# Kernel optimization log

Measured on AMD Instinct MI355X. Metric: run time of the kernel, lower is better.

The kernel has to match this reference:

```python
import jax, jax.numpy as jnp
import numpy as np

ALPHA = 0.9   # LIF membrane decay
VTH = 1.0     # LIF threshold
H = 8         # attention heads
ACH = 0.5     # acetylcholine level for thalamic gate

# Heaviside spike with fast-sigmoid surrogate gradient (standard SNN trick)
@jax.custom_vjp
def spike(v):
    return (v >= 0.0).astype(v.dtype)

def _spike_fwd(v):
    return (v >= 0.0).astype(v.dtype), v

def _spike_bwd(v, g):
    return (g / (1.0 + 2.0 * jnp.abs(v)) ** 2,)

spike.defvjp(_spike_fwd, _spike_bwd)

def lif(x):
    """Leaky-integrate-and-fire over time. x: (B,T,D) -> spikes (B,T,D). Soft reset."""
    def step(u, xt):
        u = ALPHA * u + xt
        s = spike(u - VTH)
        return u - s * VTH, s
    u0 = jnp.zeros_like(x[:, 0])
    _, s = jax.lax.scan(step, u0, jnp.swapaxes(x, 0, 1))  # scan over T
    return jnp.swapaxes(s, 0, 1)

def rwkv_wkv(k, v, w_decay, u_first):
    """Numerically-stable RWKV time-mixing recurrence. k,v: (B,T,D) -> wkv (B,T,D)."""
    w = jnp.exp(w_decay)  # positive per-channel decay
    def step(carry, kv):
        aa, bb, pp = carry
        kt, vt = kv
        ww = u_first + kt
        p = jnp.maximum(pp, ww)
        e1 = jnp.exp(pp - p); e2 = jnp.exp(ww - p)
        wkv = (e1 * aa + e2 * vt) / (e1 * bb + e2)
        ww2 = pp - w
        p2 = jnp.maximum(ww2, kt)
        e1 = jnp.exp(ww2 - p2); e2 = jnp.exp(kt - p2)
        return (e1 * aa + e2 * vt, e1 * bb + e2, p2), wkv
    B, T, D = k.shape
    init = (jnp.zeros((B, D), k.dtype), jnp.zeros((B, D), k.dtype),
            jnp.full((B, D), -1e30, k.dtype))
    _, wkv = jax.lax.scan(step, init, (jnp.swapaxes(k, 0, 1), jnp.swapaxes(v, 0, 1)))
    return jnp.swapaxes(wkv, 0, 1)


def setup_inputs() -> dict:
    key = jax.random.key(0)
    B, T, D = 4, 1024, 1024
    ks = jax.random.split(key, 16)
    s = 1.0 / np.sqrt(D)
    def W(k):
        return jax.random.normal(k, (D, D), jnp.float32) * s
    return {
        "x": jax.random.normal(ks[0], (B, T, D), jnp.float32),
        "context": jax.random.normal(ks[1], (B, T, D), jnp.float32),
        "Wg": W(ks[2]), "bg": jnp.zeros((D,), jnp.float32), "Wc": W(ks[3]),
        "Wq": W(ks[4]), "Wk": W(ks[5]), "Wv": W(ks[6]), "Wo": W(ks[7]),
        "Wm": W(ks[8]),
        "rWk": W(ks[9]), "rWv": W(ks[10]), "rWr": W(ks[11]), "rWo": W(ks[12]),
        "w_decay": jax.random.normal(ks[13], (D,), jnp.float32) * 0.1,
        "u_first": jax.random.normal(ks[14], (D,), jnp.float32) * 0.1,
        "gamma": jnp.ones((D,), jnp.float32), "beta": jnp.zeros((D,), jnp.float32),
    }


def reference(x, context, Wg, bg, Wc, Wq, Wk, Wv, Wo, Wm, rWk, rWv, rWr, rWo,
              w_decay, u_first, gamma, beta):
    B, T, D = x.shape
    dh = D // H
    # stage 1: thalamic gate (ach interpolates between pass-through and gated)
    gate = jax.nn.sigmoid(x @ Wg + bg + context @ Wc)
    gated = x * (ACH * gate + (1.0 - ACH))
    # stage 2: LIF integration (sequential over T)
    spikes2 = lif(gated)
    # stage 3: spike self-attention
    q = (spikes2 @ Wq).reshape(B, T, H, dh)
    k = (spikes2 @ Wk).reshape(B, T, H, dh)
    v = (spikes2 @ Wv).reshape(B, T, H, dh)
    scores = jnp.einsum('bthd,bshd->bhts', q, k) / np.sqrt(dh).astype(np.float32)
    attn = jax.nn.softmax(scores, axis=-1)
    attn_out = jnp.einsum('bhts,bshd->bthd', attn, v).reshape(B, T, D) @ Wo
    # stage 4: apical modulation by top-down context
    modulated = attn_out * (1.0 + jnp.tanh(context @ Wm))
    # stage 5: RWKV recurrence
    r = jax.nn.sigmoid(modulated @ rWr)
    wkv = rwkv_wkv(modulated @ rWk, modulated @ rWv, w_decay, u_first)
    recurrent = (r * wkv) @ rWo
    # stage 6: output LIF + residual + LayerNorm
    y = lif(recurrent) + spikes2
    mu = jnp.mean(y, axis=-1, keepdims=True)
    var = jnp.var(y, axis=-1, keepdims=True)
    return (y - mu) * jax.lax.rsqrt(var + 1e-5) * gamma + beta
```

## Files before the change

kernel.cpp:

```cpp
#include <hip/hip_runtime.h>
#include <hip/hip_bf16.h>
#include <math.h>

#define BDIM 4
#define TDIM 1024
#define DDIM 1024
#define DH   128
#define NELEM ((size_t)BDIM * TDIM * DDIM)

typedef __attribute__((ext_vector_type(8))) _Float16 hfrag;
typedef __attribute__((ext_vector_type(4))) float facc;

__device__ __forceinline__ void split2(float x, ushort& h1, ushort& h2) {
  const _Float16 a = (_Float16)x;
  const _Float16 b = (_Float16)((x - (float)a) * 2048.0f);
  union { _Float16 h; ushort u; } ua, ub;
  ua.h = a; ub.h = b;
  h1 = ua.u; h2 = ub.u;
}
#define INV2048 4.8828125e-4f

__device__ __forceinline__ float fexp(float x) {
  return __builtin_amdgcn_exp2f(x * 1.4426950408889634f);
}

constexpr int GM = 4096, GN = 1024, GK = 1024;
constexpr int BM = 128, BK = 32;
constexpr int BKP = 40;

__global__ __launch_bounds__(256)
void cvt_h2t(const float* __restrict__ W0, const float* __restrict__ W1,
             const float* __restrict__ W2, ushort* __restrict__ P,
             int zstride, int zkoff, int kTot) {
  __shared__ float Ls[64][68];
  const int z = blockIdx.z;
  const float* W = (z == 0) ? W0 : (z == 1 ? W1 : W2);
  ushort* Pz = P + (size_t)z * zstride;
  const size_t PS = (size_t)kTot * GN;
  const int t = threadIdx.x;
  const int k0 = blockIdx.x * 64, n0 = blockIdx.y * 64;
  const int r = t >> 4, c4 = (t & 15) << 2;
#pragma unroll
  for (int i = 0; i < 4; ++i)
    *(float4*)&Ls[r + i * 16][c4] =
        *(const float4*)(W + (size_t)(k0 + r + i * 16) * GN + n0 + c4);
  __syncthreads();
  const int n = t >> 2, kc = (t & 3) << 4;
  uint p1[8], p2[8];
#pragma unroll
  for (int jj = 0; jj < 8; ++jj) {
    const float x0 = Ls[kc + 2 * jj][n], x1 = Ls[kc + 2 * jj + 1][n];
    ushort a1, a2, b1, b2;
    split2(x0, a1, a2);
    split2(x1, b1, b2);
    p1[jj] = (uint)a1 | ((uint)b1 << 16);
    p2[jj] = (uint)a2 | ((uint)b2 << 16);
  }
  const int kk = k0 + kc + z * zkoff;
  ushort* d = Pz + (size_t)(kk >> 5) * (GN * 32) + (size_t)(n0 + n) * 32 + (kk & 31);
  *(uint4*)(d)          = *(uint4*)&p1[0];
  *(uint4*)(d + 8)      = *(uint4*)&p1[4];
  *(uint4*)(d + PS)     = *(uint4*)&p2[0];
  *(uint4*)(d + PS + 8) = *(uint4*)&p2[4];
}

template<int EPI, int AU8, int KTOT, int GATE>
__global__ __launch_bounds__(256)
void gemm_k(const void* __restrict__ A0, const void* __restrict__ A1,
            const void* __restrict__ A2, const void* __restrict__ Ak2,
            const ushort* __restrict__ pB,
            float* __restrict__ C0, float* __restrict__ C1,
            float* __restrict__ C2,
            const float* __restrict__ xg, const float* __restrict__ bgv) {
  constexpr size_t PS = (size_t)KTOT * GN;
  __shared__ ushort As[2][BM][BKP];
  __shared__ ushort Bs[2][64][BKP];
  const int tid = threadIdx.x;
  const int n   = blockIdx.x;
  const int xcd = n & 7;
  const int idx = n >> 3;
  const int by  = xcd * 4 + (idx & 3);
  const int bx  = idx >> 2;
  const int mat = bx >> 4;
  const int row0 = by * BM;
  const int col0 = (bx & 15) * 64;
  const ushort* pBm = pB + (size_t)mat * 2 * PS;
  float* C = (mat == 0) ? C0 : (mat == 1 ? C1 : C2);
  const void* Abase = (mat == 0) ? A0 : (mat == 1 ? A1 : A2);

  const int sm  = tid & 127;
  const int sk0 = (tid >> 7) << 4;

  const int wave = tid >> 6;
  const int lane = tid & 63;
  const int wrow = (wave >> 1) * 64;
  const int wcol = (wave & 1) * 32;
  const int lrow = lane & 15;
  const int kof  = (lane >> 4) * 8;

  facc accM[4][2], accS[4][2];
#pragma unroll
  for (int i = 0; i < 4; ++i)
#pragma unroll
    for (int j = 0; j < 2; ++j) { accM[i][j] = (facc)0.f; accS[i][j] = (facc)0.f; }

  float av[16];
  uint4 a8raw;
  uint4 bregs[2];

  auto gloadA = [&](int K0) {
    const void* src = Abase; int k = K0;
    if (KTOT > 1024 && K0 >= 1024) { src = Ak2; k = K0 - 1024; }
    if (AU8) {
      a8raw = *(const uint4*)((const uint8_t*)src + (size_t)(row0 + sm) * 1024 + k + sk0);
    } else {
      const float* Ap = (const float*)src + (size_t)(row0 + sm) * 1024 + k + sk0;
      *(float4*)&av[0]  = *(const float4*)(Ap);
      *(float4*)&av[4]  = *(const float4*)(Ap + 4);
      *(float4*)&av[8]  = *(const float4*)(Ap + 8);
      *(float4*)&av[12] = *(const float4*)(Ap + 12);
    }
  };
  auto gloadB = [&](int K0) {
    const int kb = K0 >> 5;
#pragma unroll
    for (int j = 0; j < 2; ++j) {
      const int u = tid + 256 * j;
      const int q = u & 3, nn = (u >> 2) & 63, p = u >> 8;
      bregs[j] = *(const uint4*)(pBm + (size_t)p * PS + (size_t)kb * (GN * 32)
                                 + (size_t)(col0 + nn) * 32 + q * 8);
    }
  };
  auto swrite = [&]() {
    if (AU8) {
      const uint w4[4] = {a8raw.x, a8raw.y, a8raw.z, a8raw.w};
      uint pk[8];
#pragma unroll
      for (int i = 0; i < 8; ++i) {
        const uint b0 = (w4[i >> 1] >> ((i & 1) * 16)) & 0xFFu;
        const uint b1 = (w4[i >> 1] >> ((i & 1) * 16 + 8)) & 0xFFu;
        pk[i] = (b0 * 0x3C00u) | ((b1 * 0x3C00u) << 16);
      }
      *(uint4*)&As[0][sm][sk0]     = *(uint4*)&pk[0];
      *(uint4*)&As[0][sm][sk0 + 8] = *(uint4*)&pk[4];
    } else {
      uint q1[8], q2[8];
#pragma unroll
      for (int i = 0; i < 8; ++i) {
        ushort a1, a2, b1, b2;
        split2(av[2 * i], a1, a2);
        split2(av[2 * i + 1], b1, b2);
        q1[i] = (uint)a1 | ((uint)b1 << 16);
        q2[i] = (uint)a2 | ((uint)b2 << 16);
      }
      *(uint4*)&As[0][sm][sk0]     = *(uint4*)&q1[0];
      *(uint4*)&As[0][sm][sk0 + 8] = *(uint4*)&q1[4];
      *(uint4*)&As[1][sm][sk0]     = *(uint4*)&q2[0];
      *(uint4*)&As[1][sm][sk0 + 8] = *(uint4*)&q2[4];
    }
#pragma unroll
    for (int j = 0; j < 2; ++j) {
      const int u = tid + 256 * j;
      const int q = u & 3, nn = (u >> 2) & 63, p = u >> 8;
      *(uint4*)&Bs[p][nn][q * 8] = bregs[j];
    }
  };

  gloadA(0); gloadB(0);
  for (int k0 = 0; k0 < KTOT; k0 += BK) {
    __syncthreads();
    swrite();
    const int kn = k0 + BK;
    if (kn < KTOT) { gloadA(kn); gloadB(kn); }
    __syncthreads();
    hfrag fb1[2], fb2[2];
#pragma unroll
    for (int f = 0; f < 2; ++f) {
      fb1[f] = *(const hfrag*)&Bs[0][wcol + f * 16 + lrow][kof];
      fb2[f] = *(const hfrag*)&Bs[1][wcol + f * 16 + lrow][kof];
    }
#pragma unroll
    for (int mi = 0; mi < 4; ++mi) {
      const hfrag a1 = *(const hfrag*)&As[0][wrow + mi * 16 + lrow][kof];
      hfrag a2;
      if (!AU8) a2 = *(const hfrag*)&As[1][wrow + mi * 16 + lrow][kof];
#pragma unroll
      for (int ni = 0; ni < 2; ++ni)
        accM[mi][ni] = __builtin_amdgcn_mfma_f32_16x16x32_f16(a1, fb1[ni], accM[mi][ni], 0, 0, 0);
#pragma unroll
      for (int ni = 0; ni < 2; ++ni) {
        accS[mi][ni] = __builtin_amdgcn_mfma_f32_16x16x32_f16(a1, fb2[ni], accS[mi][ni], 0, 0, 0);
        if (!AU8)
          accS[mi][ni] = __builtin_amdgcn_mfma_f32_16x16x32_f16(a2, fb1[ni], accS[mi][ni], 0, 0, 0);
      }
    }
  }

#pragma unroll
  for (int mi = 0; mi < 4; ++mi) {
#pragma unroll
    for (int ni = 0; ni < 2; ++ni) {
      const int rbase = row0 + wrow + mi * 16 + (lane >> 4) * 4;
      const int cc    = col0 + wcol + ni * 16 + lrow;
      float* cp = C + (size_t)rbase * GN + cc;
#pragma unroll
      for (int r = 0; r < 4; ++r) {
        float v = accM[mi][ni][r] + accS[mi][ni][r] * INV2048;
        if (EPI == 1) v += cp[(size_t)r * GN];
        if (GATE == 1) {
          const float xv = xg[(size_t)(rbase + r) * GN + cc];
          const float s  = 1.0f / (1.0f + expf(-(v + bgv[cc])));
          v = xv * (0.5f * s + 0.5f);
        }
        cp[(size_t)r * GN] = v;
      }
    }
  }
}

__device__ __forceinline__ float sigf(float z) { return 1.0f / (1.0f + expf(-z)); }

__global__ __launch_bounds__(256)
void mod_kernel(const float* __restrict__ a, const float* __restrict__ c,
                float* __restrict__ out) {
  const int i4 = blockIdx.x * 256 + threadIdx.x;
  const float4 av = ((const float4*)a)[i4];
  const float4 cv = ((const float4*)c)[i4];
  float4 r;
  r.x = av.x * (1.0f + tanhf(cv.x));
  r.y = av.y * (1.0f + tanhf(cv.y));
  r.z = av.z * (1.0f + tanhf(cv.z));
  r.w = av.w * (1.0f + tanhf(cv.w));
  ((float4*)out)[i4] = r;
}

__global__ __launch_bounds__(256)
void rmul_kernel(const float* __restrict__ rr, const float* __restrict__ wkv,
                 float* __restrict__ out) {
  const int i4 = blockIdx.x * 256 + threadIdx.x;
  const float4 rv = ((const float4*)rr)[i4];
  const float4 wv = ((const float4*)wkv)[i4];
  float4 r;
  r.x = sigf(rv.x) * wv.x;
  r.y = sigf(rv.y) * wv.y;
  r.z = sigf(rv.z) * wv.z;
  r.w = sigf(rv.w) * wv.w;
  ((float4*)out)[i4] = r;
}

__global__ __launch_bounds__(64)
void lif_u8_kernel(const float* __restrict__ x, uint8_t* __restrict__ s) {
  const int c = blockIdx.x * 64 + threadIdx.x;
  const size_t off = (size_t)(c >> 10) * TDIM * DDIM + (c & 1023);
  const float* xp = x + off;
  uint8_t* sp = s + off;
  float u = 0.f;
  float cur[32];
#pragma unroll
  for (int i = 0; i < 32; ++i) cur[i] = xp[(size_t)i * DDIM];
  for (int t = 0; t < TDIM; t += 32) {
    float nxt[32];
    if (t + 32 < TDIM) {
#pragma unroll
      for (int i = 0; i < 32; ++i) nxt[i] = xp[(size_t)(t + 32 + i) * DDIM];
    }
#pragma unroll
    for (int i = 0; i < 32; ++i) {
      u = __fadd_rn(__fmul_rn(0.9f, u), cur[i]);
      const bool fire = (u >= 1.0f);
      sp[(size_t)(t + i) * DDIM] = fire ? 1 : 0;
      if (fire) u -= 1.0f;
    }
#pragma unroll
    for (int i = 0; i < 32; ++i) cur[i] = nxt[i];
  }
}

__global__ __launch_bounds__(64)
void lif_ip_kernel(float* __restrict__ x) {
  const int c = blockIdx.x * 64 + threadIdx.x;
  const size_t off = (size_t)(c >> 10) * TDIM * DDIM + (c & 1023);
  float* xp = x + off;
  float u = 0.f;
  float cur[32];
#pragma unroll
  for (int i = 0; i < 32; ++i) cur[i] = xp[(size_t)i * DDIM];
  for (int t = 0; t < TDIM; t += 32) {
    float nxt[32];
    if (t + 32 < TDIM) {
#pragma unroll
      for (int i = 0; i < 32; ++i) nxt[i] = xp[(size_t)(t + 32 + i) * DDIM];
    }
#pragma unroll
    for (int i = 0; i < 32; ++i) {
      u = __fadd_rn(__fmul_rn(0.9f, u), cur[i]);
      const float sv = (u >= 1.0f) ? 1.0f : 0.0f;
      xp[(size_t)(t + i) * DDIM] = sv;
      u -= sv;
    }
#pragma unroll
    for (int i = 0; i < 32; ++i) cur[i] = nxt[i];
  }
}

__global__ __launch_bounds__(64)
void rwkv_kernel(const float* __restrict__ k, const float* __restrict__ v,
                 const float* __restrict__ wd, const float* __restrict__ uf,
                 float* __restrict__ out) {
  const int c = blockIdx.x * 64 + threadIdx.x;
  const int d = c & 1023;
  const size_t off = (size_t)(c >> 10) * TDIM * DDIM + d;
  const float* kp = k + off;
  const float* vp = v + off;
  float* op = out + off;
  const float w = expf(wd[d]);
  const float u = uf[d];
  float aa = 0.f, bb = 0.f, pp = -1e30f;
  float kc[16], vc[16];
#pragma unroll
  for (int i = 0; i < 16; ++i) {
    kc[i] = kp[(size_t)i * DDIM];
    vc[i] = vp[(size_t)i * DDIM];
  }
  for (int t = 0; t < TDIM; t += 16) {
    float kn[16], vn[16];
    if (t + 16 < TDIM) {
#pragma unroll
      for (int i = 0; i < 16; ++i) {
        kn[i] = kp[(size_t)(t + 16 + i) * DDIM];
        vn[i] = vp[(size_t)(t + 16 + i) * DDIM];
      }
    }
#pragma unroll
    for (int i = 0; i < 16; ++i) {
      const float kt = kc[i], vt = vc[i];
      const float ww = __fadd_rn(u, kt);
      const float p  = fmaxf(pp, ww);
      float e1 = fexp(__fsub_rn(pp, p));
      float e2 = fexp(__fsub_rn(ww, p));
      const float num = __fadd_rn(__fmul_rn(e1, aa), __fmul_rn(e2, vt));
      const float den = __fadd_rn(__fmul_rn(e1, bb), e2);
      op[(size_t)(t + i) * DDIM] = num * __builtin_amdgcn_rcpf(den);
      const float ww2 = __fsub_rn(pp, w);
      const float p2  = fmaxf(ww2, kt);
      e1 = fexp(__fsub_rn(ww2, p2));
      e2 = fexp(__fsub_rn(kt, p2));
      aa = __fadd_rn(__fmul_rn(e1, aa), __fmul_rn(e2, vt));
      bb = __fadd_rn(__fmul_rn(e1, bb), e2);
      pp = p2;
    }
#pragma unroll
    for (int i = 0; i < 16; ++i) { kc[i] = kn[i]; vc[i] = vn[i]; }
  }
}

__global__ __launch_bounds__(256)
void flash_attn(const float* __restrict__ Q, const float* __restrict__ K,
                const float* __restrict__ V, float* __restrict__ O) {
  __shared__ ushort Ks[2][32][136];
  __shared__ ushort Vt[2][128][40];
  __shared__ ushort Pl[4][2][16][40];
  const int tid = threadIdx.x;
  const int n    = blockIdx.x;
  const int xcd  = n & 7;
  const int idx  = n >> 3;
  const int qt   = idx & 15;
  const int grp4 = idx >> 4;
  const int p    = grp4 * 8 + xcd;
  const int b    = p >> 3, h = p & 7;
  const size_t base = ((size_t)b * TDIM) * DDIM + (size_t)h * DH;

  const int wave = tid >> 6;
  const int lane = tid & 63;
  const int lr   = lane & 15;
  const int g    = lane >> 4;
  const int sr   = tid >> 3;
  const int sc   = (tid & 7) * 16;
  const int vslot = (sr + 8 * (tid & 3)) & 31;

  hfrag q1[4], q2[4];
  {
    const float* Qrow = Q + base + (size_t)(qt * 64 + wave * 16 + lr) * DDIM;
#pragma unroll
    for (int s = 0; s < 4; ++s) {
      const float4 f0 = *(const float4*)(Qrow + s * 32 + g * 8);
      const float4 f1 = *(const float4*)(Qrow + s * 32 + g * 8 + 4);
      const float qf[8] = {f0.x, f0.y, f0.z, f0.w, f1.x, f1.y, f1.z, f1.w};
      union { hfrag v; ushort u[8]; } u1, u2;
#pragma unroll
      for (int j = 0; j < 8; ++j) split2(qf[j], u1.u[j], u2.u[j]);
      q1[s] = u1.v; q2[s] = u2.v;
    }
  }

  facc oM[8], oS[8];
#pragma unroll
  for (int i = 0; i < 8; ++i) { oM[i] = (facc)0.f; oS[i] = (facc)0.f; }
  float m[4] = {-INFINITY, -INFINITY, -INFINITY, -INFINITY};
  float l[4] = {0.f, 0.f, 0.f, 0.f};
  const float ISC = 0.08838834764831845f;

  float kv[16], vv[16];
  auto gload = [&](int kt0) {
    const float* Kg = K + base + (size_t)(kt0 + sr) * DDIM + sc;
    const float* Vg = V + base + (size_t)(kt0 + sr) * DDIM + sc;
    *(float4*)&kv[0]  = *(const float4*)(Kg);
    *(float4*)&kv[4]  = *(const float4*)(Kg + 4);
    *(float4*)&kv[8]  = *(const float4*)(Kg + 8);
    *(float4*)&kv[12] = *(const float4*)(Kg + 12);
    *(float4*)&vv[0]  = *(const float4*)(Vg);
    *(float4*)&vv[4]  = *(const float4*)(Vg + 4);
    *(float4*)&vv[8]  = *(const float4*)(Vg + 8);
    *(float4*)&vv[12] = *(const float4*)(Vg + 12);
  };
  gload(0);

  for (int kt0 = 0; kt0 < TDIM; kt0 += 32) {
    __syncthreads();
    {
      uint w1[8], w2[8];
#pragma unroll
      for (int i = 0; i < 8; ++i) {
        ushort a1, a2, b1, b2;
        split2(kv[2 * i], a1, a2);
        split2(kv[2 * i + 1], b1, b2);
        w1[i] = (uint)a1 | ((uint)b1 << 16);
        w2[i] = (uint)a2 | ((uint)b2 << 16);
      }
      *(uint4*)&Ks[0][sr][sc]     = *(uint4*)&w1[0];
      *(uint4*)&Ks[0][sr][sc + 8] = *(uint4*)&w1[4];
      *(uint4*)&Ks[1][sr][sc]     = *(uint4*)&w2[0];
      *(uint4*)&Ks[1][sr][sc + 8] = *(uint4*)&w2[4];
#pragma unroll
      for (int i = 0; i < 16; ++i) {
        ushort a1, a2;
        split2(vv[i], a1, a2);
        Vt[0][sc + i][vslot] = a1;
        Vt[1][sc + i][vslot] = a2;
      }
    }
    if (kt0 + 32 < TDIM) gload(kt0 + 32);
    __syncthreads();

    facc sM0 = (facc)0.f, sS0 = (facc)0.f, sM1 = (facc)0.f, sS1 = (facc)0.f;
#pragma unroll
    for (int s = 0; s < 4; ++s) {
      const int ko = s * 32 + g * 8;
      const hfrag kb10 = *(const hfrag*)&Ks[0][lr][ko];
      const hfrag kb11 = *(const hfrag*)&Ks[0][lr + 16][ko];
      const hfrag kb20 = *(const hfrag*)&Ks[1][lr][ko];
      const hfrag kb21 = *(const hfrag*)&Ks[1][lr + 16][ko];
      sM0 = __builtin_amdgcn_mfma_f32_16x16x32_f16(q1[s], kb10, sM0, 0, 0, 0);
      sS0 = __builtin_amdgcn_mfma_f32_16x16x32_f16(q1[s], kb20, sS0, 0, 0, 0);
      sS0 = __builtin_amdgcn_mfma_f32_16x16x32_f16(q2[s], kb10, sS0, 0, 0, 0);
      sM1 = __builtin_amdgcn_mfma_f32_16x16x32_f16(q1[s], kb11, sM1, 0, 0, 0);
      sS1 = __builtin_amdgcn_mfma_f32_16x16x32_f16(q1[s], kb21, sS1, 0, 0, 0);
      sS1 = __builtin_amdgcn_mfma_f32_16x16x32_f16(q2[s], kb11, sS1, 0, 0, 0);
    }

#pragma unroll
    for (int r = 0; r < 4; ++r) {
      const float sc0 = (sM0[r] + sS0[r] * INV2048) * ISC;
      const float sc1 = (sM1[r] + sS1[r] * INV2048) * ISC;
      float mx = fmaxf(sc0, sc1);
      mx = fmaxf(mx, __shfl_xor(mx, 1, 16));
      mx = fmaxf(mx, __shfl_xor(mx, 2, 16));
      mx = fmaxf(mx, __shfl_xor(mx, 4, 16));
      mx = fmaxf(mx, __shfl_xor(mx, 8, 16));
      const float mn = fmaxf(m[r], mx);
      const float rf = fexp(m[r] - mn);
      const float p0 = fexp(sc0 - mn), p1 = fexp(sc1 - mn);
      float ps = p0 + p1;
      ps += __shfl_xor(ps, 1, 16);
      ps += __shfl_xor(ps, 2, 16);
      ps += __shfl_xor(ps, 4, 16);
      ps += __shfl_xor(ps, 8, 16);
      l[r] = l[r] * rf + ps;
      m[r] = mn;
#pragma unroll
      for (int nf = 0; nf < 8; ++nf) { oM[nf][r] *= rf; oS[nf][r] *= rf; }
      ushort a1, a2;
      split2(p0, a1, a2);
      Pl[wave][0][g * 4 + r][lr] = a1;
      Pl[wave][1][g * 4 + r][lr] = a2;
      split2(p1, a1, a2);
      Pl[wave][0][g * 4 + r][lr + 16] = a1;
      Pl[wave][1][g * 4 + r][lr + 16] = a2;
    }

    const hfrag pa1 = *(const hfrag*)&Pl[wave][0][lr][g * 8];
    const hfrag pa2 = *(const hfrag*)&Pl[wave][1][lr][g * 8];
#pragma unroll
    for (int nf = 0; nf < 8; ++nf) {
      const int vs = 8 * ((g + nf) & 3);
      const hfrag vb1 = *(const hfrag*)&Vt[0][nf * 16 + lr][vs];
      const hfrag vb2 = *(const hfrag*)&Vt[1][nf * 16 + lr][vs];
      oM[nf] = __builtin_amdgcn_mfma_f32_16x16x32_f16(pa1, vb1, oM[nf], 0, 0, 0);
      oS[nf] = __builtin_amdgcn_mfma_f32_16x16x32_f16(pa1, vb2, oS[nf], 0, 0, 0);
      oS[nf] = __builtin_amdgcn_mfma_f32_16x16x32_f16(pa2, vb1, oS[nf], 0, 0, 0);
    }
  }

  float* Og = O + base + (size_t)(qt * 64 + wave * 16) * DDIM;
#pragma unroll
  for (int r = 0; r < 4; ++r) {
    const float invl = 1.0f / l[r];
    float* orow = Og + (size_t)(g * 4 + r) * DDIM;
#pragma unroll
    for (int nf = 0; nf < 8; ++nf)
      orow[nf * 16 + lr] = (oM[nf][r] + oS[nf][r] * INV2048) * invl;
  }
}

__global__ __launch_bounds__(256)
void ln_kernel(const float* __restrict__ a, const uint8_t* __restrict__ s8,
               const float* __restrict__ gamma, const float* __restrict__ beta,
               float* __restrict__ out) {
  const int row = blockIdx.x;
  const int tid = threadIdx.x;
  const size_t base = (size_t)row * DDIM;
  const float4 av = *(const float4*)(a + base + tid * 4);
  const uchar4 sv = *(const uchar4*)(s8 + base + tid * 4);
  const float y0 = av.x + (float)sv.x, y1 = av.y + (float)sv.y;
  const float y2 = av.z + (float)sv.z, y3 = av.w + (float)sv.w;
  float s = (y0 + y1) + (y2 + y3);
  float q = (y0 * y0 + y1 * y1) + (y2 * y2 + y3 * y3);
#pragma unroll
  for (int off = 1; off < 64; off <<= 1) {
    s += __shfl_xor(s, off);
    q += __shfl_xor(q, off);
  }
  __shared__ float red[8];
  const int wid = tid >> 6;
  if ((tid & 63) == 0) { red[wid * 2] = s; red[wid * 2 + 1] = q; }
  __syncthreads();
  const float ts = (red[0] + red[2]) + (red[4] + red[6]);
  const float tq = (red[1] + red[3]) + (red[5] + red[7]);
  const float mu  = ts * (1.0f / 1024.0f);
  const float var = tq * (1.0f / 1024.0f) - mu * mu;
  const float rs  = 1.0f / sqrtf(var + 1e-5f);
  const int d = tid * 4;
  const float4 gv  = *(const float4*)(gamma + d);
  const float4 btv = *(const float4*)(beta + d);
  float4 r;
  r.x = (y0 - mu) * rs * gv.x + btv.x;
  r.y = (y1 - mu) * rs * gv.y + btv.y;
  r.z = (y2 - mu) * rs * gv.z + btv.z;
  r.w = (y3 - mu) * rs * gv.w + btv.w;
  *(float4*)(out + base + d) = r;
}

extern "C" void kernel_launch(void* const* d_in, const int* in_sizes, int n_in,
                              void* d_out, int out_size, void* d_ws, size_t ws_size,
                              hipStream_t stream) {
  const float* x       = (const float*)d_in[0];
  const float* context = (const float*)d_in[1];
  const float* Wg  = (const float*)d_in[2];
  const float* bg  = (const float*)d_in[3];
  const float* Wc  = (const float*)d_in[4];
  const float* Wq  = (const float*)d_in[5];
  const float* Wk  = (const float*)d_in[6];
  const float* Wv  = (const float*)d_in[7];
  const float* Wo  = (const float*)d_in[8];
  const float* Wm  = (const float*)d_in[9];
  const float* rWk = (const float*)d_in[10];
  const float* rWv = (const float*)d_in[11];
  const float* rWr = (const float*)d_in[12];
  const float* rWo = (const float*)d_in[13];
  const float* wd  = (const float*)d_in[14];
  const float* uf  = (const float*)d_in[15];
  const float* gamma = (const float*)d_in[16];
  const float* beta  = (const float*)d_in[17];
  float* out = (float*)d_out;

  float* w  = (float*)d_ws;
  float*   bA = w;
  float*   bC = w + 1 * NELEM;
  float*   bD = w + 2 * NELEM;
  float*   bE = w + 3 * NELEM;
  uint8_t* bS = (uint8_t*)(w + 4 * NELEM);
  ushort*  pB = (ushort*)((uint8_t*)d_ws + 4 * NELEM * 4 + NELEM);

  const dim3 ew(4096);
  constexpr int M1 = 1024 * 1024;

  cvt_h2t<<<dim3(16, 16, 2), 256, 0, stream>>>(Wg, Wc, nullptr, pB, 0, 1024, 2048);
  gemm_k<0, 0, 2048, 1><<<512, 256, 0, stream>>>(x, nullptr, nullptr, context,
                                                 pB, bA, nullptr, nullptr, x, bg);
  lif_u8_kernel<<<64, 64, 0, stream>>>(bA, bS);
  cvt_h2t<<<dim3(16, 16, 3), 256, 0, stream>>>(Wq, Wk, Wv, pB, 2 * M1, 0, 1024);
  gemm_k<0, 1, 1024, 0><<<1536, 256, 0, stream>>>(bS, bS, bS, nullptr, pB,
                                                  bA, bC, bD, nullptr, nullptr);
  flash_attn<<<512, 256, 0, stream>>>(bA, bC, bD, bA);
  cvt_h2t<<<dim3(16, 16, 2), 256, 0, stream>>>(Wo, Wm, nullptr, pB, 2 * M1, 0, 1024);
  gemm_k<0, 0, 1024, 0><<<1024, 256, 0, stream>>>(bA, context, nullptr, nullptr,
                                                  pB, bC, bE, nullptr,
                                                  nullptr, nullptr);
  mod_kernel<<<ew, 256, 0, stream>>>(bC, bE, bD);
  cvt_h2t<<<dim3(16, 16, 3), 256, 0, stream>>>(rWk, rWv, rWr, pB, 2 * M1, 0, 1024);
  gemm_k<0, 0, 1024, 0><<<1536, 256, 0, stream>>>(bD, bD, bD, nullptr, pB,
                                                  bA, bC, bE, nullptr, nullptr);
  rwkv_kernel<<<64, 64, 0, stream>>>(bA, bC, wd, uf, bA);
  rmul_kernel<<<ew, 256, 0, stream>>>(bE, bA, bA);
  cvt_h2t<<<dim3(16, 16, 1), 256, 0, stream>>>(rWo, nullptr, nullptr, pB, 0, 0, 1024);
  gemm_k<0, 0, 1024, 0><<<512, 256, 0, stream>>>(bA, nullptr, nullptr, nullptr,
                                                 pB, bC, nullptr, nullptr,
                                                 nullptr, nullptr);
  lif_ip_kernel<<<64, 64, 0, stream>>>(bC);
  ln_kernel<<<4096, 256, 0, stream>>>(bC, bS, gamma, beta, out);
}
```

Measured before the change: 967.2 us.

## Double-buffer GEMM global prefetch registers to hide load latency

The GEMM main loop now keeps two sets of prefetch registers for the A and B tiles and unrolls the K loop by two. Global loads are issued two BK steps ahead instead of one, so memory latency has more time to overlap with MFMA compute. In exchange the kernel holds more registers, which may lower occupancy. The change also assumes KTOT is a multiple of 2*BK.

Result: no change. 966.1 us (-0.1%).

```diff
diff --git a/kernel.cpp b/kernel.cpp
--- a/kernel.cpp
+++ b/kernel.cpp
@@ -104,36 +104,36 @@
 #pragma unroll
     for (int j = 0; j < 2; ++j) { accM[i][j] = (facc)0.f; accS[i][j] = (facc)0.f; }
 
-  float av[16];
-  uint4 a8raw;
-  uint4 bregs[2];
-
-  auto gloadA = [&](int K0) {
+  float av0[16], av1[16];
+  uint4 a80, a81;
+  uint4 br0[2], br1[2];
+
+  auto gloadA = [&](int K0, float* avd, uint4& a8d) {
     const void* src = Abase; int k = K0;
     if (KTOT > 1024 && K0 >= 1024) { src = Ak2; k = K0 - 1024; }
     if (AU8) {
-      a8raw = *(const uint4*)((const uint8_t*)src + (size_t)(row0 + sm) * 1024 + k + sk0);
+      a8d = *(const uint4*)((const uint8_t*)src + (size_t)(row0 + sm) * 1024 + k + sk0);
     } else {
       const float* Ap = (const float*)src + (size_t)(row0 + sm) * 1024 + k + sk0;
-      *(float4*)&av[0]  = *(const float4*)(Ap);
-      *(float4*)&av[4]  = *(const float4*)(Ap + 4);
-      *(float4*)&av[8]  = *(const float4*)(Ap + 8);
-      *(float4*)&av[12] = *(const float4*)(Ap + 12);
+      *(float4*)&avd[0]  = *(const float4*)(Ap);
+      *(float4*)&avd[4]  = *(const float4*)(Ap + 4);
+      *(float4*)&avd[8]  = *(const float4*)(Ap + 8);
+      *(float4*)&avd[12] = *(const float4*)(Ap + 12);
     }
   };
-  auto gloadB = [&](int K0) {
+  auto gloadB = [&](int K0, uint4* bd) {
     const int kb = K0 >> 5;
 #pragma unroll
     for (int j = 0; j < 2; ++j) {
       const int u = tid + 256 * j;
       const int q = u & 3, nn = (u >> 2) & 63, p = u >> 8;
-      bregs[j] = *(const uint4*)(pBm + (size_t)p * PS + (size_t)kb * (GN * 32)
-                                 + (size_t)(col0 + nn) * 32 + q * 8);
+      bd[j] = *(const uint4*)(pBm + (size_t)p * PS + (size_t)kb * (GN * 32)
+                              + (size_t)(col0 + nn) * 32 + q * 8);
     }
   };
-  auto swrite = [&]() {
+  auto swrite = [&](const float* avs, const uint4& a8s, const uint4* bs) {
     if (AU8) {
-      const uint w4[4] = {a8raw.x, a8raw.y, a8raw.z, a8raw.w};
+      const uint w4[4] = {a8s.x, a8s.y, a8s.z, a8s.w};
       uint pk[8];
 #pragma unroll
       for (int i = 0; i < 8; ++i) {
@@ -148,8 +148,8 @@
 #pragma unroll
       for (int i = 0; i < 8; ++i) {
         ushort a1, a2, b1, b2;
-        split2(av[2 * i], a1, a2);
-        split2(av[2 * i + 1], b1, b2);
+        split2(avs[2 * i], a1, a2);
+        split2(avs[2 * i + 1], b1, b2);
         q1[i] = (uint)a1 | ((uint)b1 << 16);
         q2[i] = (uint)a2 | ((uint)b2 << 16);
       }
@@ -162,17 +162,10 @@
     for (int j = 0; j < 2; ++j) {
       const int u = tid + 256 * j;
       const int q = u & 3, nn = (u >> 2) & 63, p = u >> 8;
-      *(uint4*)&Bs[p][nn][q * 8] = bregs[j];
+      *(uint4*)&Bs[p][nn][q * 8] = bs[j];
     }
   };
-
-  gloadA(0); gloadB(0);
-  for (int k0 = 0; k0 < KTOT; k0 += BK) {
-    __syncthreads();
-    swrite();
-    const int kn = k0 + BK;
-    if (kn < KTOT) { gloadA(kn); gloadB(kn); }
-    __syncthreads();
+  auto compute = [&]() {
     hfrag fb1[2], fb2[2];
 #pragma unroll
     for (int f = 0; f < 2; ++f) {
@@ -194,6 +187,21 @@
           accS[mi][ni] = __builtin_amdgcn_mfma_f32_16x16x32_f16(a2, fb1[ni], accS[mi][ni], 0, 0, 0);
       }
     }
+  };
+
+  gloadA(0, av0, a80);  gloadB(0, br0);
+  gloadA(BK, av1, a81); gloadB(BK, br1);
+  for (int k0 = 0; k0 < KTOT; k0 += 2 * BK) {
+    __syncthreads();
+    swrite(av0, a80, br0);
+    if (k0 + 2 * BK < KTOT) { gloadA(k0 + 2 * BK, av0, a80); gloadB(k0 + 2 * BK, br0); }
+    __syncthreads();
+    compute();
+    __syncthreads();
+    swrite(av1, a81, br1);
+    if (k0 + 3 * BK < KTOT) { gloadA(k0 + 3 * BK, av1, a81); gloadB(k0 + 3 * BK, br1); }
+    __syncthreads();
+    compute();
   }
 
 #pragma unroll
```

## Double-buffer LDS tiles in split-fp16 GEMM to halve barriers per K step

Applied to the files above, without the earlier changes.

Shared-memory A and B tiles become double-buffered, so each iteration writes the next stage into the alternate buffer while the MFMA computes on the current one. This cuts the synchronisations per K-step from two to one and prefetches global loads two stages ahead. The cost is doubled LDS use and more live registers, which may lower occupancy.

Result: faster. 862.9 us, median of 2 (-10.8%).

```diff
diff --git a/kernel.cpp b/kernel.cpp
--- a/kernel.cpp
+++ b/kernel.cpp
@@ -73,8 +73,8 @@
             float* __restrict__ C2,
             const float* __restrict__ xg, const float* __restrict__ bgv) {
   constexpr size_t PS = (size_t)KTOT * GN;
-  __shared__ ushort As[2][BM][BKP];
-  __shared__ ushort Bs[2][64][BKP];
+  __shared__ ushort As[2][2][BM][BKP];
+  __shared__ ushort Bs[2][2][64][BKP];
   const int tid = threadIdx.x;
   const int n   = blockIdx.x;
   const int xcd = n & 7;
@@ -131,7 +131,7 @@
                                  + (size_t)(col0 + nn) * 32 + q * 8);
     }
   };
-  auto swrite = [&]() {
+  auto swrite = [&](int bi) {
     if (AU8) {
       const uint w4[4] = {a8raw.x, a8raw.y, a8raw.z, a8raw.w};
       uint pk[8];
@@ -141,8 +141,8 @@
         const uint b1 = (w4[i >> 1] >> ((i & 1) * 16 + 8)) & 0xFFu;
         pk[i] = (b0 * 0x3C00u) | ((b1 * 0x3C00u) << 16);
       }
-      *(uint4*)&As[0][sm][sk0]     = *(uint4*)&pk[0];
-      *(uint4*)&As[0][sm][sk0 + 8] = *(uint4*)&pk[4];
+      *(uint4*)&As[bi][0][sm][sk0]     = *(uint4*)&pk[0];
+      *(uint4*)&As[bi][0][sm][sk0 + 8] = *(uint4*)&pk[4];
     } else {
       uint q1[8], q2[8];
 #pragma unroll
@@ -153,37 +153,30 @@
         q1[i] = (uint)a1 | ((uint)b1 << 16);
         q2[i] = (uint)a2 | ((uint)b2 << 16);
       }
-      *(uint4*)&As[0][sm][sk0]     = *(uint4*)&q1[0];
-      *(uint4*)&As[0][sm][sk0 + 8] = *(uint4*)&q1[4];
-      *(uint4*)&As[1][sm][sk0]     = *(uint4*)&q2[0];
-      *(uint4*)&As[1][sm][sk0 + 8] = *(uint4*)&q2[4];
+      *(uint4*)&As[bi][0][sm][sk0]     = *(uint4*)&q1[0];
+      *(uint4*)&As[bi][0][sm][sk0 + 8] = *(uint4*)&q1[4];
+      *(uint4*)&As[bi][1][sm][sk0]     = *(uint4*)&q2[0];
+      *(uint4*)&As[bi][1][sm][sk0 + 8] = *(uint4*)&q2[4];
     }
 #pragma unroll
     for (int j = 0; j < 2; ++j) {
       const int u = tid + 256 * j;
       const int q = u & 3, nn = (u >> 2) & 63, p = u >> 8;
-      *(uint4*)&Bs[p][nn][q * 8] = bregs[j];
+      *(uint4*)&Bs[bi][p][nn][q * 8] = bregs[j];
     }
   };
-
-  gloadA(0); gloadB(0);
-  for (int k0 = 0; k0 < KTOT; k0 += BK) {
-    __syncthreads();
-    swrite();
-    const int kn = k0 + BK;
-    if (kn < KTOT) { gloadA(kn); gloadB(kn); }
-    __syncthreads();
+  auto compute = [&](int bi) {
     hfrag fb1[2], fb2[2];
 #pragma unroll
     for (int f = 0; f < 2; ++f) {
-      fb1[f] = *(const hfrag*)&Bs[0][wcol + f * 16 + lrow][kof];
-      fb2[f] = *(const hfrag*)&Bs[1][wcol + f * 16 + lrow][kof];
+      fb1[f] = *(const hfrag*)&Bs[bi][0][wcol + f * 16 + lrow][kof];
+      fb2[f] = *(const hfrag*)&Bs[bi][1][wcol + f * 16 + lrow][kof];
     }
 #pragma unroll
     for (int mi = 0; mi < 4; ++mi) {
-      const hfrag a1 = *(const hfrag*)&As[0][wrow + mi * 16 + lrow][kof];
+      const hfrag a1 = *(const hfrag*)&As[bi][0][wrow + mi * 16 + lrow][kof];
       hfrag a2;
-      if (!AU8) a2 = *(const hfrag*)&As[1][wrow + mi * 16 + lrow][kof];
+      if (!AU8) a2 = *(const hfrag*)&As[bi][1][wrow + mi * 16 + lrow][kof];
 #pragma unroll
       for (int ni = 0; ni < 2; ++ni)
         accM[mi][ni] = __builtin_amdgcn_mfma_f32_16x16x32_f16(a1, fb1[ni], accM[mi][ni], 0, 0, 0);
@@ -194,6 +187,19 @@
           accS[mi][ni] = __builtin_amdgcn_mfma_f32_16x16x32_f16(a2, fb1[ni], accS[mi][ni], 0, 0, 0);
       }
     }
+  };
+
+  constexpr int NK = KTOT / BK;
+  gloadA(0); gloadB(0);
+  swrite(0);
+  gloadA(BK); gloadB(BK);
+  __syncthreads();
+  for (int ks = 0; ks < NK; ++ks) {
+    const int cur = ks & 1;
+    if (ks + 1 < NK) swrite(cur ^ 1);
+    if (ks + 2 < NK) { gloadA((ks + 2) * BK); gloadB((ks + 2) * BK); }
+    compute(cur);
+    __syncthreads();
   }
 
 #pragma unroll
```
